# Performance work log

Measured on AMD Instinct MI355X. Metric: run time of the kernel, lower is better.

The kernel has to match this reference:

```python
import jax, jax.numpy as jnp
import numpy as np

B, N, M, D, H = 8, 2048, 2048, 512, 8


def setup_inputs() -> dict:
    key = jax.random.key(0)
    ks = jax.random.split(key, 12)
    std = D ** (-0.5)
    inp = {
        "k": jax.random.normal(ks[0], (B, N, D), jnp.float32),
        "v": jax.random.normal(ks[1], (B, N, D), jnp.float32),
        "q": jax.random.normal(ks[2], (B, M, D), jnp.float32),
        # per-head projections, stacked over the head axis: [H, D, D]
        "Wk": jax.random.normal(ks[3], (H, D, D), jnp.float32) * std,
        "bk": jax.random.normal(ks[4], (H, D), jnp.float32) * 0.01,
        "Wv": jax.random.normal(ks[5], (H, D, D), jnp.float32) * std,
        "bv": jax.random.normal(ks[6], (H, D), jnp.float32) * 0.01,
        "Wq": jax.random.normal(ks[7], (H, D, D), jnp.float32) * std,
        "bq": jax.random.normal(ks[8], (H, D), jnp.float32) * 0.01,
        # final linear: input ordering is (hidden_dim, head) flattened -> H*D
        "Wo": jax.random.normal(ks[9], (H * D, D), jnp.float32) * (H * D) ** (-0.5),
        "bo": jax.random.normal(ks[10], (D,), jnp.float32) * 0.01,
    }
    return inp


def reference(k, v, q, Wk, bk, Wv, bv, Wq, bq, Wo, bo):
    # Per-head linear projections (torch loops over heads; here batched over h).
    # nn.Linear computes x @ W.T + b; Wk here stores W.T directly as [H, D, D].
    k_ = jnp.einsum("bnd,hde->bhne", k, Wk) + bk[None, :, None, :]  # [B,H,N,D]
    v_ = jnp.einsum("bnd,hde->bhne", v, Wv) + bv[None, :, None, :]  # [B,H,N,D]
    q_ = jnp.einsum("bmd,hde->bhme", q, Wq) + bq[None, :, None, :]  # [B,H,M,D]

    scale = D ** 0.5
    scores = jnp.einsum("bhmd,bhnd->bhmn", q_, k_) / scale  # [B,H,M,N]
    weights = jax.nn.softmax(scores, axis=-1)
    out = jnp.einsum("bhmn,bhnd->bhmd", weights, v_)  # [B,H,M,D]

    # torch: stack(outs, dim=-1) -> [B,M,D,H], then view -> [B,M,D*H]
    outs = jnp.transpose(out, (0, 2, 3, 1)).reshape(B, M, D * H)
    # matching flatten order (d-major, h-minor) requires Wo rows ordered d*H+h;
    # setup generates Wo random so any consistent ordering is faithful.
    rep = outs @ Wo + bo  # [B,M,D]
    return rep
```

## Files before the change

kernel.cpp:

```cpp
#include <hip/hip_runtime.h>
#include <hip/hip_bf16.h>
#include <cstdint>
#include <cstddef>

typedef __bf16 bf16x8 __attribute__((ext_vector_type(8)));
typedef __bf16 bf16x4 __attribute__((ext_vector_type(4)));
typedef float floatx4 __attribute__((ext_vector_type(4)));

#define MFMA16(a, b, c) __builtin_amdgcn_mfma_f32_16x16x32_bf16((a), (b), (c), 0, 0, 0)

__device__ __forceinline__ void load_lds16(const __bf16* g, __bf16* l) {
  __builtin_amdgcn_global_load_lds(
      (const __attribute__((address_space(1))) uint32_t*)(g),
      (__attribute__((address_space(3))) uint32_t*)(l), 16, 0, 0);
}

__global__ __launch_bounds__(256) void tw_t(const float* __restrict__ W,
                                            __bf16* __restrict__ Wt, float scale) {
  __shared__ float tile[64][65];
  int h = blockIdx.z, d0 = blockIdx.y * 64, e0 = blockIdx.x * 64;
  int tx = threadIdx.x & 15, ty = threadIdx.x >> 4;
  const float* src = W + ((size_t)h * 512 + d0) * 512 + e0;
#pragma unroll
  for (int j = 0; j < 4; ++j) {
    int dd = ty + j * 16;
    float4 f = *(const float4*)&src[(size_t)dd * 512 + tx * 4];
    tile[dd][tx * 4 + 0] = f.x; tile[dd][tx * 4 + 1] = f.y;
    tile[dd][tx * 4 + 2] = f.z; tile[dd][tx * 4 + 3] = f.w;
  }
  __syncthreads();
  __bf16* dst = Wt + ((size_t)h * 512 + e0) * 512 + d0;
#pragma unroll
  for (int j = 0; j < 4; ++j) {
    int ee = ty + j * 16;
    bf16x4 v;
#pragma unroll
    for (int x = 0; x < 4; ++x) v[x] = (__bf16)(tile[tx * 4 + x][ee] * scale);
    *(bf16x4*)&dst[(size_t)ee * 512 + tx * 4] = v;
  }
}

__global__ __launch_bounds__(256) void wo_t(const float* __restrict__ Wo,
                                            __bf16* __restrict__ Wot) {
  __shared__ float tile[64][65];
  int h = blockIdx.z, d0 = blockIdx.y * 64, e0 = blockIdx.x * 64;
  int tx = threadIdx.x & 15, ty = threadIdx.x >> 4;
#pragma unroll
  for (int j = 0; j < 4; ++j) {
    int dd = ty + j * 16;
    float4 f = *(const float4*)&Wo[(size_t)((d0 + dd) * 8 + h) * 512 + e0 + tx * 4];
    tile[dd][tx * 4 + 0] = f.x; tile[dd][tx * 4 + 1] = f.y;
    tile[dd][tx * 4 + 2] = f.z; tile[dd][tx * 4 + 3] = f.w;
  }
  __syncthreads();
#pragma unroll
  for (int j = 0; j < 4; ++j) {
    int ee = ty + j * 16;
    bf16x4 v;
#pragma unroll
    for (int x = 0; x < 4; ++x) v[x] = (__bf16)tile[tx * 4 + x][ee];
    *(bf16x4*)&Wot[(size_t)(e0 + ee) * 4096 + h * 512 + d0 + tx * 4] = v;
  }
}

template <int EPI, bool AF32>
__global__ __launch_bounds__(256) void gemm_bt(const void* __restrict__ Ap,
                                               const __bf16* __restrict__ Bt,
                                               const float* __restrict__ bias,
                                               void* __restrict__ Cout,
                                               int N, int K, float bscale) {
  __shared__ __align__(16) __bf16 sA[128][72];
  __shared__ __align__(16) __bf16 sB[128][72];
  const int tid = threadIdx.x;
  const int lane = tid & 63;
  const int wave = tid >> 6;
  const int lr = lane & 15;
  const int lq = lane >> 4;
  const int wm = (wave >> 1) * 64;
  const int wn = (wave & 1) * 64;
  const int bx = blockIdx.x, by = blockIdx.y;
  const int srow = tid >> 3;
  const int scol = (tid & 7) << 3;

  const floatx4 z4 = {0.f, 0.f, 0.f, 0.f};
  floatx4 acc[4][4];
#pragma unroll
  for (int i = 0; i < 4; ++i)
#pragma unroll
    for (int j = 0; j < 4; ++j) acc[i][j] = z4;

  const size_t abase = (size_t)(by * 128) * K;
  const size_t bbase = (size_t)(bx * 128) * K;

  for (int k0 = 0; k0 < K; k0 += 64) {
#pragma unroll
    for (int p = 0; p < 4; ++p) {
      int row = p * 32 + srow;
      if (AF32) {
        const float* A = (const float*)Ap;
        float4 f0 = *(const float4*)&A[abase + (size_t)row * K + k0 + scol];
        float4 f1 = *(const float4*)&A[abase + (size_t)row * K + k0 + scol + 4];
        bf16x8 v;
        v[0] = (__bf16)f0.x; v[1] = (__bf16)f0.y; v[2] = (__bf16)f0.z; v[3] = (__bf16)f0.w;
        v[4] = (__bf16)f1.x; v[5] = (__bf16)f1.y; v[6] = (__bf16)f1.z; v[7] = (__bf16)f1.w;
        *(bf16x8*)&sA[row][scol] = v;
      } else {
        const __bf16* A = (const __bf16*)Ap;
        *(bf16x8*)&sA[row][scol] = *(const bf16x8*)&A[abase + (size_t)row * K + k0 + scol];
      }
      *(bf16x8*)&sB[row][scol] = *(const bf16x8*)&Bt[bbase + (size_t)row * K + k0 + scol];
    }
    __syncthreads();
#pragma unroll
    for (int ks = 0; ks < 2; ++ks) {
      bf16x8 af[4], bfr[4];
#pragma unroll
      for (int mt = 0; mt < 4; ++mt)
        af[mt] = *(const bf16x8*)&sA[wm + mt * 16 + lr][ks * 32 + lq * 8];
#pragma unroll
      for (int nt = 0; nt < 4; ++nt)
        bfr[nt] = *(const bf16x8*)&sB[wn + nt * 16 + lr][ks * 32 + lq * 8];
#pragma unroll
      for (int mt = 0; mt < 4; ++mt)
#pragma unroll
        for (int nt = 0; nt < 4; ++nt) acc[mt][nt] = MFMA16(af[mt], bfr[nt], acc[mt][nt]);
    }
    __syncthreads();
  }

#pragma unroll
  for (int mt = 0; mt < 4; ++mt) {
#pragma unroll
    for (int nt = 0; nt < 4; ++nt) {
      int col = bx * 128 + wn + nt * 16 + lr;
      int row0 = by * 128 + wm + mt * 16 + lq * 4;
      float bcol = bias[col] * bscale;
      if (EPI == 0) {
        __bf16* dst = (__bf16*)Cout;
        int h = col >> 9, e = col & 511;
#pragma unroll
        for (int r = 0; r < 4; ++r) {
          int row = row0 + r;
          int b = row >> 11, m = row & 2047;
          dst[((size_t)((b << 3) | h) * 2048 + m) * 512 + e] = (__bf16)(acc[mt][nt][r] + bcol);
        }
      } else if (EPI == 1) {
        __bf16* dst = (__bf16*)Cout;
        int h = col >> 9, e = col & 511;
        int b = row0 >> 11, n = row0 & 2047;
        bf16x4 pk;
#pragma unroll
        for (int r = 0; r < 4; ++r) pk[r] = (__bf16)(acc[mt][nt][r] + bcol);
        *(bf16x4*)&dst[((size_t)((b << 3) | h) * 512 + e) * 2048 + n] = pk;
      } else {
        float* dst = (float*)Cout;
#pragma unroll
        for (int r = 0; r < 4; ++r) {
          int row = row0 + r;
          dst[(size_t)row * N + col] = acc[mt][nt][r] + bcol;
        }
      }
    }
  }
}

__global__ __launch_bounds__(512, 2) void attn_kernel(const __bf16* __restrict__ Qp,
                                                      const __bf16* __restrict__ Kp,
                                                      const __bf16* __restrict__ Vt,
                                                      __bf16* __restrict__ Outs) {
  __shared__ __align__(16) __bf16 kls[2][32 * 512];
  __shared__ __align__(16) __bf16 vls[2][512 * 32];
  __shared__ __align__(16) __bf16 pls[2][128 * 40];
  __shared__ __align__(16) float l_red[128];
  const int tid = threadIdx.x;
  const int lane = tid & 63;
  const int wave = tid >> 6;
  const int lr = lane & 15;
  const int lq = lane >> 4;
  const int blk = blockIdx.x;
  const int bh = blk >> 4;
  const int mblk = blk & 15;
  const int qrow0 = wave * 16;
  const int m0 = mblk * 128 + qrow0;
  const int e0 = wave * 64;
  const __bf16* Qb = Qp + (size_t)bh * (2048 * 512);
  const __bf16* Kb = Kp + (size_t)bh * (2048 * 512);
  const __bf16* Vb = Vt + (size_t)bh * (512 * 2048);

  int gK[4], gV[4];
#pragma unroll
  for (int i = 0; i < 4; ++i) {
    int q = i * 512 + tid;
    int rK = q >> 6;
    gK[i] = rK * 512 + ((q & 63) ^ (rK & 7)) * 8;
    int eV = q >> 2;
    gV[i] = eV * 2048 + ((q & 3) ^ (eV & 3)) * 8;
  }

  bf16x8 qf[16];
#pragma unroll
  for (int ks = 0; ks < 16; ++ks)
    qf[ks] = *(const bf16x8*)&Qb[(size_t)(m0 + lr) * 512 + ks * 32 + lq * 8];

  const floatx4 z4 = {0.f, 0.f, 0.f, 0.f};
  floatx4 o[8][4];
#pragma unroll
  for (int mt = 0; mt < 8; ++mt)
#pragma unroll
    for (int et = 0; et < 4; ++et) o[mt][et] = z4;
  float lsum[4] = {0.f, 0.f, 0.f, 0.f};

  auto pv_step = [&](const __bf16* pc, const __bf16* vc) {
    bf16x8 vf[4];
#pragma unroll
    for (int et = 0; et < 4; ++et) {
      int e = e0 + et * 16 + lr;
      vf[et] = *(const bf16x8*)&vc[e * 32 + ((lq ^ (e & 3)) * 8)];
    }
#pragma unroll
    for (int mt = 0; mt < 8; ++mt) {
      bf16x8 pf = *(const bf16x8*)&pc[(mt * 16 + lr) * 40 + lq * 8];
#pragma unroll
      for (int et = 0; et < 4; ++et) o[mt][et] = MFMA16(pf, vf[et], o[mt][et]);
    }
  };

#pragma unroll
  for (int i = 0; i < 4; ++i) load_lds16(Kb + gK[i], &kls[0][i * 4096 + wave * 512]);
  __syncthreads();

  for (int t = 0; t < 64; ++t) {
    const int cur = t & 1;
    if (t < 63) {
      const __bf16* kg = Kb + (size_t)(t + 1) * (32 * 512);
#pragma unroll
      for (int i = 0; i < 4; ++i)
        load_lds16(kg + gK[i], &kls[cur ^ 1][i * 4096 + wave * 512]);
    }
    {
      const __bf16* vg = Vb + t * 32;
#pragma unroll
      for (int i = 0; i < 4; ++i)
        load_lds16(vg + gV[i], &vls[cur][i * 4096 + wave * 512]);
    }
    floatx4 s0 = z4, s1 = z4;
    const __bf16* kc = kls[cur];
#pragma unroll
    for (int ks = 0; ks < 16; ++ks) {
      int cidx = ((ks * 4 + lq) ^ (lr & 7)) * 8;
      bf16x8 k0 = *(const bf16x8*)&kc[lr * 512 + cidx];
      bf16x8 k1 = *(const bf16x8*)&kc[(16 + lr) * 512 + cidx];
      s0 = MFMA16(qf[ks], k0, s0);
      s1 = MFMA16(qf[ks], k1, s1);
    }
#pragma unroll
    for (int r = 0; r < 4; ++r) {
      float p0 = __expf(s0[r]);
      float p1 = __expf(s1[r]);
      lsum[r] += p0 + p1;
      pls[cur][(qrow0 + lq * 4 + r) * 40 + lr] = (__bf16)p0;
      pls[cur][(qrow0 + lq * 4 + r) * 40 + 16 + lr] = (__bf16)p1;
    }
    if (t > 0) pv_step(pls[cur ^ 1], vls[cur ^ 1]);
    __syncthreads();
  }
  pv_step(pls[1], vls[1]);

#pragma unroll
  for (int r = 0; r < 4; ++r) {
    float s = lsum[r];
    s += __shfl_xor(s, 1);
    s += __shfl_xor(s, 2);
    s += __shfl_xor(s, 4);
    s += __shfl_xor(s, 8);
    lsum[r] = s;
  }
  if (lr == 0) {
#pragma unroll
    for (int r = 0; r < 4; ++r) l_red[qrow0 + lq * 4 + r] = lsum[r];
  }
  __syncthreads();

  int b = bh >> 3, h = bh & 7;
#pragma unroll
  for (int mt = 0; mt < 8; ++mt) {
    float4 lv = *(const float4*)&l_red[mt * 16 + lq * 4];
    float invr[4] = {1.0f / lv.x, 1.0f / lv.y, 1.0f / lv.z, 1.0f / lv.w};
    size_t rowbase = ((size_t)b * 2048 + mblk * 128 + mt * 16 + lq * 4) * 4096 + h * 512 + e0;
#pragma unroll
    for (int et = 0; et < 4; ++et)
#pragma unroll
      for (int r = 0; r < 4; ++r)
        Outs[rowbase + (size_t)r * 4096 + et * 16 + lr] = (__bf16)(o[mt][et][r] * invr[r]);
  }
}

extern "C" void kernel_launch(void* const* d_in, const int* in_sizes, int n_in,
                              void* d_out, int out_size, void* d_ws, size_t ws_size,
                              hipStream_t stream) {
  (void)in_sizes; (void)n_in; (void)out_size;
  const float* kin = (const float*)d_in[0];
  const float* vin = (const float*)d_in[1];
  const float* qin = (const float*)d_in[2];
  const float* Wk  = (const float*)d_in[3];
  const float* bk  = (const float*)d_in[4];
  const float* Wv  = (const float*)d_in[5];
  const float* bv  = (const float*)d_in[6];
  const float* Wq  = (const float*)d_in[7];
  const float* bq  = (const float*)d_in[8];
  const float* Wo  = (const float*)d_in[9];
  const float* bo  = (const float*)d_in[10];
  float* out = (float*)d_out;
  char* ws = (char*)d_ws;

  const float scale = 0.044194173824159216f;

  const size_t SZ_W = (size_t)4096 * 512 * 2;
  const size_t SZ_B = (size_t)8 * 2048 * 512 * 2;
  const size_t FIXED = 4 * SZ_W;

  int nb = 1;
  if (ws_size >= FIXED + 8 * 4 * SZ_B) nb = 8;
  else if (ws_size >= FIXED + 4 * 4 * SZ_B) nb = 4;
  else if (ws_size >= FIXED + 2 * 4 * SZ_B) nb = 2;

  __bf16* Wkt = (__bf16*)(ws);
  __bf16* Wvt = (__bf16*)(ws + SZ_W);
  __bf16* Wqt = (__bf16*)(ws + 2 * SZ_W);
  __bf16* Wot = (__bf16*)(ws + 3 * SZ_W);
  char* chunkbase = ws + FIXED;
  __bf16* kproj = (__bf16*)(chunkbase);
  __bf16* qproj = (__bf16*)(chunkbase + (size_t)nb * SZ_B);
  __bf16* vt    = (__bf16*)(chunkbase + (size_t)nb * 2 * SZ_B);
  __bf16* outs  = (__bf16*)(chunkbase + (size_t)nb * 3 * SZ_B);

  tw_t<<<dim3(8, 8, 8), dim3(256), 0, stream>>>(Wk, Wkt, 1.0f);
  tw_t<<<dim3(8, 8, 8), dim3(256), 0, stream>>>(Wv, Wvt, 1.0f);
  tw_t<<<dim3(8, 8, 8), dim3(256), 0, stream>>>(Wq, Wqt, scale);
  wo_t<<<dim3(8, 8, 8), dim3(256), 0, stream>>>(Wo, Wot);

  for (int b0 = 0; b0 < 8; b0 += nb) {
    const float* kc = kin + (size_t)b0 * 2048 * 512;
    const float* vc = vin + (size_t)b0 * 2048 * 512;
    const float* qc = qin + (size_t)b0 * 2048 * 512;
    gemm_bt<0, true><<<dim3(32, nb * 16), dim3(256), 0, stream>>>(kc, Wkt, bk, (void*)kproj, 4096, 512, 1.0f);
    gemm_bt<0, true><<<dim3(32, nb * 16), dim3(256), 0, stream>>>(qc, Wqt, bq, (void*)qproj, 4096, 512, scale);
    gemm_bt<1, true><<<dim3(32, nb * 16), dim3(256), 0, stream>>>(vc, Wvt, bv, (void*)vt, 4096, 512, 1.0f);
    attn_kernel<<<dim3(nb * 128), dim3(512), 0, stream>>>(qproj, kproj, vt, outs);
    gemm_bt<2, false><<<dim3(4, nb * 16), dim3(256), 0, stream>>>(
        (void*)outs, Wot, bo, (void*)(out + (size_t)b0 * 2048 * 512), 512, 4096, 1.0f);
  }
}
```

Before: 1.658 ms.

## Split QK^T over head-dim halves across wave pairs and exchange partial scores via LDS

Each wave now computes scores for two 16-row query tiles over half of the head dimension, so every K fragment loaded from LDS feeds two MFMAs and LDS reads of K per wave are halved. Partial scores are exchanged between paired waves through a new LDS buffer and summed before the exponential. The P/V pipeline is restructured: V is prefetched together with K a step ahead, P is single-buffered, and the PV step runs within the same iteration. The cost is two extra block barriers per iteration and the loss of the previous overlap of softmax with the prior tile's PV.

```diff
diff --git a/kernel.cpp b/kernel.cpp
--- a/kernel.cpp
+++ b/kernel.cpp
@@ -170,7 +170,8 @@
                                                       __bf16* __restrict__ Outs) {
   __shared__ __align__(16) __bf16 kls[2][32 * 512];
   __shared__ __align__(16) __bf16 vls[2][512 * 32];
-  __shared__ __align__(16) __bf16 pls[2][128 * 40];
+  __shared__ __align__(16) __bf16 pls[128 * 40];
+  __shared__ __align__(16) floatx4 sx[2][8][64];
   __shared__ __align__(16) float l_red[128];
   const int tid = threadIdx.x;
   const int lane = tid & 63;
@@ -180,9 +181,11 @@
   const int blk = blockIdx.x;
   const int bh = blk >> 4;
   const int mblk = blk & 15;
-  const int qrow0 = wave * 16;
-  const int m0 = mblk * 128 + qrow0;
+  const int rp = (wave & 3) * 2;
+  const int dh = wave >> 2;
+  const int fg = rp + dh;
   const int e0 = wave * 64;
+  const int mbase = mblk * 128;
   const __bf16* Qb = Qp + (size_t)bh * (2048 * 512);
   const __bf16* Kb = Kp + (size_t)bh * (2048 * 512);
   const __bf16* Vb = Vt + (size_t)bh * (512 * 2048);
@@ -197,10 +200,13 @@
     gV[i] = eV * 2048 + ((q & 3) ^ (eV & 3)) * 8;
   }
 
-  bf16x8 qf[16];
-#pragma unroll
-  for (int ks = 0; ks < 16; ++ks)
-    qf[ks] = *(const bf16x8*)&Qb[(size_t)(m0 + lr) * 512 + ks * 32 + lq * 8];
+  bf16x8 qf[2][8];
+#pragma unroll
+  for (int j = 0; j < 2; ++j)
+#pragma unroll
+    for (int ks = 0; ks < 8; ++ks)
+      qf[j][ks] = *(const bf16x8*)&Qb[(size_t)(mbase + (rp + j) * 16 + lr) * 512 +
+                                      dh * 256 + ks * 32 + lq * 8];
 
   const floatx4 z4 = {0.f, 0.f, 0.f, 0.f};
   floatx4 o[8][4];
@@ -210,61 +216,70 @@
     for (int et = 0; et < 4; ++et) o[mt][et] = z4;
   float lsum[4] = {0.f, 0.f, 0.f, 0.f};
 
-  auto pv_step = [&](const __bf16* pc, const __bf16* vc) {
-    bf16x8 vf[4];
-#pragma unroll
-    for (int et = 0; et < 4; ++et) {
-      int e = e0 + et * 16 + lr;
-      vf[et] = *(const bf16x8*)&vc[e * 32 + ((lq ^ (e & 3)) * 8)];
-    }
-#pragma unroll
-    for (int mt = 0; mt < 8; ++mt) {
-      bf16x8 pf = *(const bf16x8*)&pc[(mt * 16 + lr) * 40 + lq * 8];
-#pragma unroll
-      for (int et = 0; et < 4; ++et) o[mt][et] = MFMA16(pf, vf[et], o[mt][et]);
-    }
-  };
-
-#pragma unroll
-  for (int i = 0; i < 4; ++i) load_lds16(Kb + gK[i], &kls[0][i * 4096 + wave * 512]);
+#pragma unroll
+  for (int i = 0; i < 4; ++i) {
+    load_lds16(Kb + gK[i], &kls[0][i * 4096 + wave * 512]);
+    load_lds16(Vb + gV[i], &vls[0][i * 4096 + wave * 512]);
+  }
   __syncthreads();
 
   for (int t = 0; t < 64; ++t) {
     const int cur = t & 1;
+    floatx4 s[2][2];
+    s[0][0] = z4; s[0][1] = z4; s[1][0] = z4; s[1][1] = z4;
+    const __bf16* kc = kls[cur];
+#pragma unroll
+    for (int ks = 0; ks < 8; ++ks) {
+      int cidx = ((dh * 32 + ks * 4 + lq) ^ (lr & 7)) * 8;
+      bf16x8 k0 = *(const bf16x8*)&kc[lr * 512 + cidx];
+      bf16x8 k1 = *(const bf16x8*)&kc[(16 + lr) * 512 + cidx];
+      s[0][0] = MFMA16(qf[0][ks], k0, s[0][0]);
+      s[0][1] = MFMA16(qf[0][ks], k1, s[0][1]);
+      s[1][0] = MFMA16(qf[1][ks], k0, s[1][0]);
+      s[1][1] = MFMA16(qf[1][ks], k1, s[1][1]);
+    }
+    sx[0][wave][lane] = s[dh ^ 1][0];
+    sx[1][wave][lane] = s[dh ^ 1][1];
+    __syncthreads();
+    {
+      floatx4 q0 = sx[0][wave ^ 4][lane];
+      floatx4 q1 = sx[1][wave ^ 4][lane];
+#pragma unroll
+      for (int r = 0; r < 4; ++r) {
+        float p0 = __expf(s[dh][0][r] + q0[r]);
+        float p1 = __expf(s[dh][1][r] + q1[r]);
+        lsum[r] += p0 + p1;
+        pls[(fg * 16 + lq * 4 + r) * 40 + lr] = (__bf16)p0;
+        pls[(fg * 16 + lq * 4 + r) * 40 + 16 + lr] = (__bf16)p1;
+      }
+    }
+    __syncthreads();
     if (t < 63) {
       const __bf16* kg = Kb + (size_t)(t + 1) * (32 * 512);
-#pragma unroll
-      for (int i = 0; i < 4; ++i)
+      const __bf16* vg = Vb + (t + 1) * 32;
+#pragma unroll
+      for (int i = 0; i < 4; ++i) {
         load_lds16(kg + gK[i], &kls[cur ^ 1][i * 4096 + wave * 512]);
+        load_lds16(vg + gV[i], &vls[cur ^ 1][i * 4096 + wave * 512]);
+      }
     }
     {
-      const __bf16* vg = Vb + t * 32;
-#pragma unroll
-      for (int i = 0; i < 4; ++i)
-        load_lds16(vg + gV[i], &vls[cur][i * 4096 + wave * 512]);
-    }
-    floatx4 s0 = z4, s1 = z4;
-    const __bf16* kc = kls[cur];
-#pragma unroll
-    for (int ks = 0; ks < 16; ++ks) {
-      int cidx = ((ks * 4 + lq) ^ (lr & 7)) * 8;
-      bf16x8 k0 = *(const bf16x8*)&kc[lr * 512 + cidx];
-      bf16x8 k1 = *(const bf16x8*)&kc[(16 + lr) * 512 + cidx];
-      s0 = MFMA16(qf[ks], k0, s0);
-      s1 = MFMA16(qf[ks], k1, s1);
-    }
-#pragma unroll
-    for (int r = 0; r < 4; ++r) {
-      float p0 = __expf(s0[r]);
-      float p1 = __expf(s1[r]);
-      lsum[r] += p0 + p1;
-      pls[cur][(qrow0 + lq * 4 + r) * 40 + lr] = (__bf16)p0;
-      pls[cur][(qrow0 + lq * 4 + r) * 40 + 16 + lr] = (__bf16)p1;
-    }
-    if (t > 0) pv_step(pls[cur ^ 1], vls[cur ^ 1]);
-    __syncthreads();
-  }
-  pv_step(pls[1], vls[1]);
+      const __bf16* vc = vls[cur];
+      bf16x8 vf[4];
+#pragma unroll
+      for (int et = 0; et < 4; ++et) {
+        int e = e0 + et * 16 + lr;
+        vf[et] = *(const bf16x8*)&vc[e * 32 + ((lq ^ (e & 3)) * 8)];
+      }
+#pragma unroll
+      for (int mt = 0; mt < 8; ++mt) {
+        bf16x8 pf = *(const bf16x8*)&pls[(mt * 16 + lr) * 40 + lq * 8];
+#pragma unroll
+        for (int et = 0; et < 4; ++et) o[mt][et] = MFMA16(pf, vf[et], o[mt][et]);
+      }
+    }
+    __syncthreads();
+  }
 
 #pragma unroll
   for (int r = 0; r < 4; ++r) {
@@ -277,7 +292,7 @@
   }
   if (lr == 0) {
 #pragma unroll
-    for (int r = 0; r < 4; ++r) l_red[qrow0 + lq * 4 + r] = lsum[r];
+    for (int r = 0; r < 4; ++r) l_red[fg * 16 + lq * 4 + r] = lsum[r];
   }
   __syncthreads();
 
@@ -286,7 +301,7 @@
   for (int mt = 0; mt < 8; ++mt) {
     float4 lv = *(const float4*)&l_red[mt * 16 + lq * 4];
     float invr[4] = {1.0f / lv.x, 1.0f / lv.y, 1.0f / lv.z, 1.0f / lv.w};
-    size_t rowbase = ((size_t)b * 2048 + mblk * 128 + mt * 16 + lq * 4) * 4096 + h * 512 + e0;
+    size_t rowbase = ((size_t)b * 2048 + mbase + mt * 16 + lq * 4) * 4096 + h * 512 + e0;
 #pragma unroll
     for (int et = 0; et < 4; ++et)
 #pragma unroll
```

Result: slower. 2.399 ms (+44.7%).
